# Kernel optimization log

Measured on AMD Instinct MI355X. Metric: run time of the kernel, lower is better.

## Reference

```python
import jax, jax.numpy as jnp
import numpy as np

TOP_K = 3
COMMIT = 0.25


def setup_inputs() -> dict:
    key = jax.random.key(0)
    k1, k2, k3 = jax.random.split(key, 3)
    features = jax.random.normal(k1, (197, 128, 768), dtype=jnp.float32)
    class_emb = jax.random.normal(k2, (4096, 768), dtype=jnp.float32)
    feat_emb = jax.random.normal(k3, (4096, 768), dtype=jnp.float32)
    return {"features": features, "class_emb": class_emb, "feat_emb": feat_emb}


def _vq(x, emb):
    # x: [A, B, C]; emb: [K, C]
    A, B, C = x.shape
    K = emb.shape[0]
    N = A * B
    flat = x.reshape(N, C)
    d = (jnp.sum(flat * flat, axis=1, keepdims=True)
         + jnp.sum(emb * emb, axis=1)
         - 2.0 * flat @ emb.T)                      # [N, K]
    _, idx = jax.lax.top_k(-d, TOP_K)               # smallest-k indices [N, k]
    quant = emb[idx].reshape(A, B, TOP_K, C)        # gather codewords
    xr = x[:, :, None, :]                           # [A, B, 1, C]
    e_latent_loss = jnp.mean((jax.lax.stop_gradient(quant) - jnp.broadcast_to(xr, quant.shape)) ** 2)
    loss = COMMIT * e_latent_loss
    q_st = xr + jax.lax.stop_gradient(quant - xr)   # straight-through [A,B,k,C]
    # avg_probs: mean over rows of the top-k one-hot encodings (rows sum to k)
    counts = jnp.zeros((K,), x.dtype).at[idx.reshape(-1)].add(1.0)
    avg_probs = counts / N
    perplexity = jnp.exp(-jnp.sum(avg_probs * jnp.log(avg_probs + 1e-10)))
    return loss, q_st, perplexity, avg_probs, idx.reshape(A, B, TOP_K), d.reshape(A, B, K)


def _forward(features, class_emb, feat_emb):
    cl_loss, cl_q, cl_perp, cl_avg, cl_idx, cl_dist = _vq(features[0:1], class_emb)
    ft_loss, ft_q, ft_perp, ft_avg, ft_idx, ft_dist = _vq(features[1:], feat_emb)
    Kc = class_emb.shape[0]
    Kf = feat_emb.shape[0]
    FMAX = jnp.float32(np.finfo(np.float32).max)
    B = features.shape[1]
    T = features.shape[0] - 1
    cl_dist_p = jnp.concatenate([cl_dist, jnp.full((1, B, Kf), FMAX, jnp.float32)], axis=-1)
    ft_dist_p = jnp.concatenate([jnp.full((T, B, Kc), FMAX, jnp.float32), ft_dist], axis=-1)
    distances = jnp.concatenate([cl_dist_p, ft_dist_p], axis=0)          # [T+1, B, Kc+Kf]
    encoding_indices = jnp.concatenate([cl_idx, ft_idx + Kc], axis=0)    # [T+1, B, k]
    quantized = jnp.concatenate([cl_q, ft_q], axis=0)                    # [T+1, B, k, C]
    loss = ft_loss + cl_loss
    return (loss, quantized, cl_perp, ft_perp, cl_avg, ft_avg, encoding_indices, distances)


def reference(features, class_emb, feat_emb):
    return _forward(features, class_emb, feat_emb)
```

## Files before the change

### kernel.cpp

```cpp
#include <hip/hip_runtime.h>
#include <math.h>

#define DEVFN __device__ __forceinline__

typedef short  s16x8 __attribute__((ext_vector_type(8)));
typedef float  f32x4 __attribute__((ext_vector_type(4)));

constexpr int C     = 768;
constexpr int NROWS = 25216;
constexpr int NCL   = 128;
constexpr int KCB   = 4096;
constexpr int KOUT  = 8192;
constexpr int TK    = 3;
constexpr int NT    = 24;
constexpr int MT    = 197;
constexpr int NTB   = 16;

constexpr long long QUANT_OFF  = 1;
constexpr long long QUANT_SZ   = (long long)NROWS * TK * C;
constexpr long long CLPERP_OFF = QUANT_OFF + QUANT_SZ;
constexpr long long FTPERP_OFF = CLPERP_OFF + 1;
constexpr long long CLAVG_OFF  = FTPERP_OFF + 1;
constexpr long long FTAVG_OFF  = CLAVG_OFF + KCB;
constexpr long long ENC_OFF    = FTAVG_OFF + KCB;
constexpr long long DIST_OFF   = ENC_OFF + (long long)NROWS * TK;

constexpr size_t XS_ELE = (size_t)MT * NT * 4096;
constexpr size_t ES_ELE = (size_t)2 * NTB * NT * 8192;

constexpr float FMAXV = 3.4028234663852886e38f;
constexpr float PADV  = 3.3895313892515355e38f;

DEVFN void gload_lds16(const void* g, void* l) {
    __builtin_amdgcn_global_load_lds(
        (const __attribute__((address_space(1))) unsigned*)g,
        (__attribute__((address_space(3))) unsigned*)l, 16, 0, 0);
}

DEVFN bool better(float v, int i, float bv, int bi) {
    return (v < bv) | ((v == bv) & (i < bi));
}
DEVFN void ins3(float v, int i, float& v0, int& i0, float& v1, int& i1, float& v2, int& i2) {
    const bool b0 = better(v, i, v0, i0);
    const bool b1 = better(v, i, v1, i1);
    const bool b2 = better(v, i, v2, i2);
    const float nv1 = b0 ? v0 : (b1 ? v : v1);
    const int   ni1 = b0 ? i0 : (b1 ? i : i1);
    const float nv2 = b1 ? v1 : (b2 ? v : v2);
    const int   ni2 = b1 ? i1 : (b2 ? i : i2);
    v0 = b0 ? v : v0;  i0 = b0 ? i : i0;
    v1 = nv1;          i1 = ni1;
    v2 = nv2;          i2 = ni2;
}

__global__ void init_kernel(float* counts) {
    int i = blockIdx.x * blockDim.x + threadIdx.x;
    if (i < KOUT) counts[i] = 0.0f;
}

__global__ void norms_kernel(const float* __restrict__ X,
                             const float* __restrict__ CE,
                             const float* __restrict__ FE,
                             float* __restrict__ xnorm,
                             float* __restrict__ enorm) {
    int row  = blockIdx.x * 4 + (threadIdx.x >> 6);
    int lane = threadIdx.x & 63;
    const int TOT = NROWS + 2 * KCB;
    if (row >= TOT) return;
    const float* src; float* dst;
    if (row < NROWS) { src = X + (long long)row * C; dst = xnorm + row; }
    else {
        int r = row - NROWS;
        src = (r < KCB) ? (CE + (long long)r * C) : (FE + (long long)(r - KCB) * C);
        dst = enorm + r;
    }
    const float4* p = (const float4*)src;
    float s = 0.f;
    for (int j = lane; j < C / 4; j += 64) {
        float4 v = p[j];
        s += v.x*v.x + v.y*v.y + v.z*v.z + v.w*v.w;
    }
    for (int o = 32; o > 0; o >>= 1) s += __shfl_down(s, o);
    if (lane == 0) *dst = s;
}

__global__ __launch_bounds__(256)
void presplit_kernel(const float* __restrict__ X,
                     const float* __restrict__ CE,
                     const float* __restrict__ FE,
                     short* __restrict__ XsH, short* __restrict__ XsL,
                     short* __restrict__ EsH, short* __restrict__ EsL) {
    const int b = blockIdx.x;
    const float* src; char* dH; char* dL; int nrr;
    if (b < MT * NT) {
        const int tile = b / NT, ks = b % NT;
        src = X + (size_t)tile * 128 * C + ks * 32;
        dH = (char*)(XsH + (size_t)b * 4096);
        dL = (char*)(XsL + (size_t)b * 4096);
        nrr = 2;
    } else {
        const int bb = b - MT * NT;
        const int book = bb / (NTB * NT);
        const int rem  = bb % (NTB * NT);
        const int tile = rem / NT, ks = rem % NT;
        src = (book ? FE : CE) + (size_t)tile * 256 * C + ks * 32;
        dH = (char*)(EsH + (size_t)bb * 8192);
        dL = (char*)(EsL + (size_t)bb * 8192);
        nrr = 4;
    }
    const int tid = threadIdx.x;
    const int row = tid >> 2, oc = tid & 3;
    for (int rr = 0; rr < nrr; ++rr) {
        const int r = row + rr * 64;
        const float* s = src + (size_t)r * C + oc * 8;
        float4 v0 = *(const float4*)s;
        float4 v1 = *(const float4*)(s + 4);
        float f[8] = {v0.x, v0.y, v0.z, v0.w, v1.x, v1.y, v1.z, v1.w};
        s16x8 hi, lo;
        #pragma unroll
        for (int q = 0; q < 8; ++q) {
            unsigned u = __float_as_uint(f[q]);
            hi[q] = (short)(u >> 16);
            lo[q] = (short)(__float_as_uint(f[q] - __uint_as_float(u & 0xffff0000u)) >> 16);
        }
        const int off = (r * 64 + oc * 16) ^ ((r & 7) << 4);
        *(s16x8*)(dH + off) = hi;
        *(s16x8*)(dL + off) = lo;
    }
}

__global__ __launch_bounds__(512, 2)
void gemm_dist_kernel(const short* __restrict__ XsH, const short* __restrict__ XsL,
                      const short* __restrict__ EsH, const short* __restrict__ EsL,
                      const float* __restrict__ xnorm,
                      const float* __restrict__ enorm,
                      float* __restrict__ dist) {
    __shared__ __align__(16) char smem[2 * 49152];

    const int orig = blockIdx.y * gridDim.x + blockIdx.x;
    const int wg   = (orig & 7) * 394 + (orig >> 3);
    const int mt = wg >> 4, nt = wg & 15;

    const int m0 = mt * 128, n0 = nt * 256;
    const int colbase = (mt == 0) ? 0 : KCB;
    const int btile = ((mt == 0) ? 0 : NTB) + nt;
    const int tid = threadIdx.x, l = tid & 63, w = tid >> 6;
    const int wy = w >> 2, wx = w & 3;

    const char* sbase[6]; size_t sstr[6]; int ldso[6];
    #pragma unroll
    for (int i = 0; i < 6; ++i) {
        const int wc = w * 6 + i;
        const char* pb; int within; size_t st;
        if (wc < 8)       { pb = (const char*)XsH + (size_t)mt * NT * 8192;     within = wc * 1024;        st = 8192;  }
        else if (wc < 16) { pb = (const char*)XsL + (size_t)mt * NT * 8192;     within = (wc - 8) * 1024;  st = 8192;  }
        else if (wc < 32) { pb = (const char*)EsH + (size_t)btile * NT * 16384; within = (wc - 16) * 1024; st = 16384; }
        else              { pb = (const char*)EsL + (size_t)btile * NT * 16384; within = (wc - 32) * 1024; st = 16384; }
        sbase[i] = pb + within + l * 16;
        sstr[i]  = st;
        ldso[i]  = wc * 1024 + l * 16;
    }
    auto STAGE = [&](int buf, int t) {
        #pragma unroll
        for (int i = 0; i < 6; ++i)
            gload_lds16(sbase[i] + (size_t)t * sstr[i], smem + buf * 49152 + ldso[i]);
    };

    const int arow = wy * 64 + (l & 15);
    const int brow = wx * 64 + (l & 15);
    const int abase = (arow * 64 + ((l >> 4) * 16)) ^ ((l & 7) << 4);
    const int bbase = (brow * 64 + ((l >> 4) * 16)) ^ ((l & 7) << 4);

    f32x4 acc[4][4];
    #pragma unroll
    for (int i = 0; i < 4; ++i)
        #pragma unroll
        for (int j = 0; j < 4; ++j) acc[i][j] = (f32x4){0.f, 0.f, 0.f, 0.f};

    STAGE(0, 0);
    int cur = 0;
    for (int t = 0; t < NT; ++t) {
        if (t + 1 < NT) {
            STAGE(cur ^ 1, t + 1);
            asm volatile("s_waitcnt vmcnt(6)" ::: "memory");
        } else {
            asm volatile("s_waitcnt vmcnt(0)" ::: "memory");
        }
        __builtin_amdgcn_s_barrier();
        __builtin_amdgcn_sched_barrier(0);

        const char* sb = smem + cur * 49152;
        s16x8 ah[4], bh[4];
        #pragma unroll
        for (int i = 0; i < 4; ++i) ah[i] = *(const s16x8*)(sb + abase + i * 1024);
        #pragma unroll
        for (int j = 0; j < 4; ++j) bh[j] = *(const s16x8*)(sb + 16384 + bbase + j * 1024);
        #pragma unroll
        for (int i = 0; i < 4; ++i)
            #pragma unroll
            for (int j = 0; j < 4; ++j)
                acc[i][j] = __builtin_amdgcn_mfma_f32_16x16x32_bf16(ah[i], bh[j], acc[i][j], 0, 0, 0);

        s16x8 al[4];
        #pragma unroll
        for (int i = 0; i < 4; ++i) al[i] = *(const s16x8*)(sb + 8192 + abase + i * 1024);
        #pragma unroll
        for (int i = 0; i < 4; ++i)
            #pragma unroll
            for (int j = 0; j < 4; ++j)
                acc[i][j] = __builtin_amdgcn_mfma_f32_16x16x32_bf16(al[i], bh[j], acc[i][j], 0, 0, 0);

        s16x8 bl[4];
        #pragma unroll
        for (int j = 0; j < 4; ++j) bl[j] = *(const s16x8*)(sb + 32768 + bbase + j * 1024);
        #pragma unroll
        for (int i = 0; i < 4; ++i)
            #pragma unroll
            for (int j = 0; j < 4; ++j)
                acc[i][j] = __builtin_amdgcn_mfma_f32_16x16x32_bf16(ah[i], bl[j], acc[i][j], 0, 0, 0);

        __builtin_amdgcn_sched_barrier(0);
        asm volatile("s_waitcnt lgkmcnt(0)" ::: "memory");
        __builtin_amdgcn_s_barrier();
        cur ^= 1;
    }

    const int lr = (l >> 4) * 4;
    const int lc = l & 15;
    float en_r[4];
    #pragma unroll
    for (int j = 0; j < 4; ++j) en_r[j] = enorm[colbase + n0 + wx * 64 + j * 16 + lc];
    #pragma unroll
    for (int i = 0; i < 4; ++i) {
        #pragma unroll
        for (int q = 0; q < 4; ++q) {
            const int gm = m0 + wy * 64 + i * 16 + lr + q;
            const float xnv = xnorm[gm];
            float* o = dist + (long long)gm * KOUT + colbase + n0 + wx * 64 + lc;
            #pragma unroll
            for (int j = 0; j < 4; ++j)
                o[j * 16] = (xnv + en_r[j]) - 2.0f * acc[i][j][q];
        }
    }

    const int padbase = (mt == 0) ? KCB : 0;
    for (int r2 = w; r2 < 128; r2 += 8) {
        float* p = dist + (long long)(m0 + r2) * KOUT + padbase + n0;
        p[l] = PADV; p[l + 64] = PADV; p[l + 128] = PADV; p[l + 192] = PADV;
    }
}

__global__ __launch_bounds__(256, 4)
void topk_kernel(const float* __restrict__ dist,
                 int* __restrict__ idxbuf,
                 float* __restrict__ out,
                 float* __restrict__ counts) {
    int rb = blockIdx.x * 4 + (threadIdx.x >> 6);
    if (rb >= NROWS) return;
    const int row = NROWS - 1 - rb;
    const int lane = threadIdx.x & 63;
    const int colbase = (row < NCL) ? 0 : KCB;
    const float* d = dist + (long long)row * KOUT + colbase;
    float v0 = FMAXV, v1 = FMAXV, v2 = FMAXV;
    int   i0 = 0x7fffffff, i1 = 0x7fffffff, i2 = 0x7fffffff;

    const float4* dv = (const float4*)(d + 1);

    float4 b[16];
    #pragma unroll
    for (int it = 0; it < 15; ++it) b[it] = dv[it * 64 + lane];
    const bool hasLast = (960 + lane) < 1023;
    b[15] = hasLast ? dv[960 + lane]
                    : (float4){FMAXV, FMAXV, FMAXV, FMAXV};
    #pragma unroll
    for (int it = 0; it < 15; ++it) {
        const int k = 1 + (it * 64 + lane) * 4;
        ins3(b[it].x, k,     v0, i0, v1, i1, v2, i2);
        ins3(b[it].y, k + 1, v0, i0, v1, i1, v2, i2);
        ins3(b[it].z, k + 2, v0, i0, v1, i1, v2, i2);
        ins3(b[it].w, k + 3, v0, i0, v1, i1, v2, i2);
    }
    {
        const int k = 1 + (960 + lane) * 4;
        const int kk = hasLast ? k : 0x7ffffff0;
        ins3(b[15].x, kk,     v0, i0, v1, i1, v2, i2);
        ins3(b[15].y, kk + 1, v0, i0, v1, i1, v2, i2);
        ins3(b[15].z, kk + 2, v0, i0, v1, i1, v2, i2);
        ins3(b[15].w, kk + 3, v0, i0, v1, i1, v2, i2);
    }
    if (lane < 4) {
        const int k = (lane == 0) ? 0 : 4092 + lane;
        ins3(d[k], k, v0, i0, v1, i1, v2, i2);
    }

    #pragma unroll
    for (int off = 32; off > 0; off >>= 1) {
        float w0 = __shfl_down(v0, off), w1 = __shfl_down(v1, off), w2 = __shfl_down(v2, off);
        int   j0 = __shfl_down(i0, off), j1 = __shfl_down(i1, off), j2 = __shfl_down(i2, off);
        ins3(w0, j0, v0, i0, v1, i1, v2, i2);
        ins3(w1, j1, v0, i0, v1, i1, v2, i2);
        ins3(w2, j2, v0, i0, v1, i1, v2, i2);
    }
    if (lane == 0) {
        long long rt = (long long)row * TK;
        idxbuf[rt + 0] = i0; idxbuf[rt + 1] = i1; idxbuf[rt + 2] = i2;
        out[ENC_OFF + rt + 0] = (float)(i0 + colbase);
        out[ENC_OFF + rt + 1] = (float)(i1 + colbase);
        out[ENC_OFF + rt + 2] = (float)(i2 + colbase);
        atomicAdd(&counts[i0 + colbase], 1.0f);
        atomicAdd(&counts[i1 + colbase], 1.0f);
        atomicAdd(&counts[i2 + colbase], 1.0f);
    }
}

__global__ __launch_bounds__(192)
void gather_kernel(const float* __restrict__ X,
                   const float* __restrict__ CE,
                   const float* __restrict__ FE,
                   const int* __restrict__ idxbuf,
                   float* __restrict__ out,
                   float* __restrict__ partials) {
    const int row = blockIdx.x;
    const int tid = threadIdx.x;
    const float4 xv = ((const float4*)(X + (size_t)row * C))[tid];
    const float* Ebase = (row < NCL) ? CE : FE;
    const long long rt0 = (long long)row * TK;
    float s = 0.f;
    #pragma unroll
    for (int t = 0; t < TK; ++t) {
        const int id = idxbuf[rt0 + t];
        const float4 ev = ((const float4*)(Ebase + (size_t)id * C))[tid];
        const float d0 = ev.x - xv.x, d1 = ev.y - xv.y, d2 = ev.z - xv.z, d3 = ev.w - xv.w;
        s += d0*d0 + d1*d1 + d2*d2 + d3*d3;
        float* q = out + QUANT_OFF + (rt0 + t) * C + tid * 4;
        q[0] = xv.x + d0; q[1] = xv.y + d1; q[2] = xv.z + d2; q[3] = xv.w + d3;
    }
    #pragma unroll
    for (int o = 32; o > 0; o >>= 1) s += __shfl_down(s, o);
    __shared__ float red[3];
    const int lane = tid & 63, w = tid >> 6;
    if (lane == 0) red[w] = s;
    __syncthreads();
    if (tid == 0) partials[row] = red[0] + red[1] + red[2];
}

__global__ void finalize_kernel(const float* __restrict__ counts,
                                const float* __restrict__ partials,
                                float* __restrict__ out) {
    __shared__ float  red[2][4];
    __shared__ double redd[2][4];
    int tid = threadIdx.x, lane = tid & 63, w = tid >> 6;
    float ecl = 0.f, eft = 0.f;
    for (int i = tid; i < KCB; i += blockDim.x) {
        float p = counts[i] * (1.0f / 128.0f);
        out[CLAVG_OFF + i] = p;
        ecl += p * logf(p + 1e-10f);
        float qv = counts[KCB + i] * (1.0f / 25088.0f);
        out[FTAVG_OFF + i] = qv;
        eft += qv * logf(qv + 1e-10f);
    }
    double scl = 0.0, sft = 0.0;
    for (int i = tid; i < NROWS; i += blockDim.x) {
        double v = (double)partials[i];
        if (i < NCL) scl += v; else sft += v;
    }
    for (int o = 32; o > 0; o >>= 1) {
        ecl += __shfl_down(ecl, o); eft += __shfl_down(eft, o);
        scl += __shfl_down(scl, o); sft += __shfl_down(sft, o);
    }
    if (lane == 0) { red[0][w] = ecl; red[1][w] = eft; redd[0][w] = scl; redd[1][w] = sft; }
    __syncthreads();
    if (tid == 0) {
        float tcl = red[0][0] + red[0][1] + red[0][2] + red[0][3];
        float tft = red[1][0] + red[1][1] + red[1][2] + red[1][3];
        double dcl = redd[0][0] + redd[0][1] + redd[0][2] + redd[0][3];
        double dft = redd[1][0] + redd[1][1] + redd[1][2] + redd[1][3];
        out[CLPERP_OFF] = expf(-tcl);
        out[FTPERP_OFF] = expf(-tft);
        float cl_loss = 0.25f * (float)(dcl / 294912.0);
        float ft_loss = 0.25f * (float)(dft / 57802752.0);
        out[0] = ft_loss + cl_loss;
    }
}

extern "C" void kernel_launch(void* const* d_in, const int* in_sizes, int n_in,
                              void* d_out, int out_size, void* d_ws, size_t ws_size,
                              hipStream_t stream) {
    const float* X  = (const float*)d_in[0];
    const float* CE = (const float*)d_in[1];
    const float* FE = (const float*)d_in[2];
    float* out = (float*)d_out;

    float* ws_f   = (float*)d_ws;
    float* xnorm  = ws_f;
    float* enorm  = ws_f + NROWS;
    float* counts = ws_f + NROWS + KOUT;
    int*   idxbuf = (int*)(ws_f + NROWS + 2 * KOUT);
    float* ssepart = xnorm;
    float* dist   = out + DIST_OFF;

    short* XsH = (short*)(out + 4);
    short* XsL = XsH + XS_ELE;
    short* EsH = XsL + XS_ELE;
    short* EsL = EsH + ES_ELE;

    init_kernel<<<32, 256, 0, stream>>>(counts);
    norms_kernel<<<(NROWS + 2 * KCB) / 4, 256, 0, stream>>>(X, CE, FE, xnorm, enorm);
    presplit_kernel<<<MT * NT + 2 * NTB * NT, 256, 0, stream>>>(X, CE, FE, XsH, XsL, EsH, EsL);
    gemm_dist_kernel<<<dim3(NTB, MT), 512, 0, stream>>>(XsH, XsL, EsH, EsL, xnorm, enorm, dist);
    topk_kernel<<<NROWS / 4, 256, 0, stream>>>(dist, idxbuf, out, counts);
    gather_kernel<<<NROWS, 192, 0, stream>>>(X, CE, FE, idxbuf, out, ssepart);
    finalize_kernel<<<1, 256, 0, stream>>>(counts, ssepart, out);
}
```

Before: 1.766 ms.

## Fuse partial top-3 selection into GEMM epilogue and merge partials in small kernel

The GEMM epilogue now keeps a running top-3 over each lane's distance values and reduces it across 16 lanes with shuffles. Each row gets 64 partial triples, one per 64-column slice, written to scratch space carved from the output buffer. The separate top-k kernel no longer re-reads 4096 distances per row from global memory; it only merges those 64 partial triples. This removes a large read of the distance matrix, at the cost of extra shuffles and comparisons plus register pressure in the GEMM epilogue.

```diff
diff --git a/kernel.cpp b/kernel.cpp
--- a/kernel.cpp
+++ b/kernel.cpp
@@ -27,6 +27,7 @@
 
 constexpr size_t XS_ELE = (size_t)MT * NT * 4096;
 constexpr size_t ES_ELE = (size_t)2 * NTB * NT * 8192;
+constexpr size_t PV_ELE = (size_t)NROWS * 64 * 3;
 
 constexpr float FMAXV = 3.4028234663852886e38f;
 constexpr float PADV  = 3.3895313892515355e38f;
@@ -134,7 +135,9 @@
                       const short* __restrict__ EsH, const short* __restrict__ EsL,
                       const float* __restrict__ xnorm,
                       const float* __restrict__ enorm,
-                      float* __restrict__ dist) {
+                      float* __restrict__ dist,
+                      float* __restrict__ pval,
+                      int* __restrict__ pidx) {
     __shared__ __align__(16) char smem[2 * 49152];
 
     const int orig = blockIdx.y * gridDim.x + blockIdx.x;
@@ -227,6 +230,7 @@
 
     const int lr = (l >> 4) * 4;
     const int lc = l & 15;
+    const int halfid = nt * 4 + wx;
     float en_r[4];
     #pragma unroll
     for (int j = 0; j < 4; ++j) en_r[j] = enorm[colbase + n0 + wx * 64 + j * 16 + lc];
@@ -237,9 +241,27 @@
             const int gm = m0 + wy * 64 + i * 16 + lr + q;
             const float xnv = xnorm[gm];
             float* o = dist + (long long)gm * KOUT + colbase + n0 + wx * 64 + lc;
+            float tv0 = FMAXV, tv1 = FMAXV, tv2 = FMAXV;
+            int   ti0 = 0x7fffffff, ti1 = 0x7fffffff, ti2 = 0x7fffffff;
             #pragma unroll
-            for (int j = 0; j < 4; ++j)
-                o[j * 16] = (xnv + en_r[j]) - 2.0f * acc[i][j][q];
+            for (int j = 0; j < 4; ++j) {
+                const float dvv = (xnv + en_r[j]) - 2.0f * acc[i][j][q];
+                o[j * 16] = dvv;
+                ins3(dvv, n0 + wx * 64 + j * 16 + lc, tv0, ti0, tv1, ti1, tv2, ti2);
+            }
+            #pragma unroll
+            for (int off = 8; off > 0; off >>= 1) {
+                float u0 = __shfl_down(tv0, off), u1 = __shfl_down(tv1, off), u2 = __shfl_down(tv2, off);
+                int   j0 = __shfl_down(ti0, off), j1 = __shfl_down(ti1, off), j2 = __shfl_down(ti2, off);
+                ins3(u0, j0, tv0, ti0, tv1, ti1, tv2, ti2);
+                ins3(u1, j1, tv0, ti0, tv1, ti1, tv2, ti2);
+                ins3(u2, j2, tv0, ti0, tv1, ti1, tv2, ti2);
+            }
+            if (lc == 0) {
+                const long long pb = ((long long)gm * 64 + halfid) * 3;
+                pval[pb + 0] = tv0; pval[pb + 1] = tv1; pval[pb + 2] = tv2;
+                pidx[pb + 0] = ti0; pidx[pb + 1] = ti1; pidx[pb + 2] = ti2;
+            }
         }
     }
 
@@ -250,49 +272,19 @@
     }
 }
 
-__global__ __launch_bounds__(256, 4)
-void topk_kernel(const float* __restrict__ dist,
-                 int* __restrict__ idxbuf,
-                 float* __restrict__ out,
-                 float* __restrict__ counts) {
-    int rb = blockIdx.x * 4 + (threadIdx.x >> 6);
-    if (rb >= NROWS) return;
-    const int row = NROWS - 1 - rb;
+__global__ __launch_bounds__(256)
+void topk_merge_kernel(const float* __restrict__ pval,
+                       const int* __restrict__ pidx,
+                       int* __restrict__ idxbuf,
+                       float* __restrict__ out,
+                       float* __restrict__ counts) {
+    int row = blockIdx.x * 4 + (threadIdx.x >> 6);
+    if (row >= NROWS) return;
     const int lane = threadIdx.x & 63;
     const int colbase = (row < NCL) ? 0 : KCB;
-    const float* d = dist + (long long)row * KOUT + colbase;
-    float v0 = FMAXV, v1 = FMAXV, v2 = FMAXV;
-    int   i0 = 0x7fffffff, i1 = 0x7fffffff, i2 = 0x7fffffff;
-
-    const float4* dv = (const float4*)(d + 1);
-
-    float4 b[16];
-    #pragma unroll
-    for (int it = 0; it < 15; ++it) b[it] = dv[it * 64 + lane];
-    const bool hasLast = (960 + lane) < 1023;
-    b[15] = hasLast ? dv[960 + lane]
-                    : (float4){FMAXV, FMAXV, FMAXV, FMAXV};
-    #pragma unroll
-    for (int it = 0; it < 15; ++it) {
-        const int k = 1 + (it * 64 + lane) * 4;
-        ins3(b[it].x, k,     v0, i0, v1, i1, v2, i2);
-        ins3(b[it].y, k + 1, v0, i0, v1, i1, v2, i2);
-        ins3(b[it].z, k + 2, v0, i0, v1, i1, v2, i2);
-        ins3(b[it].w, k + 3, v0, i0, v1, i1, v2, i2);
-    }
-    {
-        const int k = 1 + (960 + lane) * 4;
-        const int kk = hasLast ? k : 0x7ffffff0;
-        ins3(b[15].x, kk,     v0, i0, v1, i1, v2, i2);
-        ins3(b[15].y, kk + 1, v0, i0, v1, i1, v2, i2);
-        ins3(b[15].z, kk + 2, v0, i0, v1, i1, v2, i2);
-        ins3(b[15].w, kk + 3, v0, i0, v1, i1, v2, i2);
-    }
-    if (lane < 4) {
-        const int k = (lane == 0) ? 0 : 4092 + lane;
-        ins3(d[k], k, v0, i0, v1, i1, v2, i2);
-    }
-
+    const long long pb = ((long long)row * 64 + lane) * 3;
+    float v0 = pval[pb + 0], v1 = pval[pb + 1], v2 = pval[pb + 2];
+    int   i0 = pidx[pb + 0], i1 = pidx[pb + 1], i2 = pidx[pb + 2];
     #pragma unroll
     for (int off = 32; off > 0; off >>= 1) {
         float w0 = __shfl_down(v0, off), w1 = __shfl_down(v1, off), w2 = __shfl_down(v2, off);
@@ -403,12 +395,15 @@
     short* XsL = XsH + XS_ELE;
     short* EsH = XsL + XS_ELE;
     short* EsL = EsH + ES_ELE;
+    float* pval = (float*)(EsL + ES_ELE);
+    int*   pidx = (int*)(pval + PV_ELE);
 
     init_kernel<<<32, 256, 0, stream>>>(counts);
     norms_kernel<<<(NROWS + 2 * KCB) / 4, 256, 0, stream>>>(X, CE, FE, xnorm, enorm);
     presplit_kernel<<<MT * NT + 2 * NTB * NT, 256, 0, stream>>>(X, CE, FE, XsH, XsL, EsH, EsL);
-    gemm_dist_kernel<<<dim3(NTB, MT), 512, 0, stream>>>(XsH, XsL, EsH, EsL, xnorm, enorm, dist);
-    topk_kernel<<<NROWS / 4, 256, 0, stream>>>(dist, idxbuf, out, counts);
+    gemm_dist_kernel<<<dim3(NTB, MT), 512, 0, stream>>>(XsH, XsL, EsH, EsL, xnorm, enorm,
+                                                        dist, pval, pidx);
+    topk_merge_kernel<<<NROWS / 4, 256, 0, stream>>>(pval, pidx, idxbuf, out, counts);
     gather_kernel<<<NROWS, 192, 0, stream>>>(X, CE, FE, idxbuf, out, ssepart);
     finalize_kernel<<<1, 256, 0, stream>>>(counts, ssepart, out);
 }
```

New measurement: 1.941 ms. +9.9%, slower.
